# Kernel optimization log

Hardware: AMD Instinct MI355X
Metric: run time of the kernel (lower is better)

Reference implementation:

```python
import jax, jax.numpy as jnp
import numpy as np

TOPK = 13
NUM_CLASSES = 80
ALPHA = 1.0
BETA = 6.0
EPS = 1e-9
BS, NA, NMAX = 16, 8400, 64
IMG = 640


def _anchor_grid():
    pts = []
    for s in (8, 16, 32):
        n = IMG // s
        yv, xv = jnp.meshgrid(jnp.arange(n, dtype=jnp.float32), jnp.arange(n, dtype=jnp.float32), indexing='ij')
        pts.append(jnp.stack([(xv + 0.5) * s, (yv + 0.5) * s], -1).reshape(-1, 2))
    return jnp.concatenate(pts, 0)  # (8400, 2)


def setup_inputs() -> dict:
    key = jax.random.key(0)
    ks = jax.random.split(key, 6)
    pd_scores = jax.nn.sigmoid(jax.random.normal(ks[0], (BS, NA, NUM_CLASSES), jnp.float32))
    # predicted circles: centers in image, radii in [4, 68]
    pxy = jax.random.uniform(ks[1], (BS, NA, 2), jnp.float32) * IMG
    pr = jax.random.uniform(ks[1], (BS, NA, 1), jnp.float32) * 64.0 + 4.0
    pd_circles = jnp.concatenate([pxy, pr], -1)
    anc_points = _anchor_grid()
    gt_labels = jax.random.randint(ks[2], (BS, NMAX, 1), 0, NUM_CLASSES, jnp.int32)
    gxy = jax.random.uniform(ks[3], (BS, NMAX, 2), jnp.float32) * IMG
    gr = jax.random.uniform(ks[3], (BS, NMAX, 1), jnp.float32) * 64.0 + 8.0
    gt_bboxes = jnp.concatenate([gxy, gr], -1)  # circles (x, y, r)
    n_valid = jax.random.randint(ks[4], (BS, 1), 8, NMAX + 1)
    mask_gt = (jnp.arange(NMAX)[None, :] < n_valid).astype(jnp.float32)[..., None]
    return {"pd_scores": pd_scores, "pd_circles": pd_circles, "anc_points": anc_points,
            "gt_labels": gt_labels, "gt_bboxes": gt_bboxes, "mask_gt": mask_gt}


def circle_iou(c1, c2, eps):
    # c1, c2: broadcastable (..., 3) = (x, y, r); IoU of two discs via lens area.
    d = jnp.sqrt(jnp.sum((c1[..., :2] - c2[..., :2]) ** 2, -1) + eps)
    r1, r2 = c1[..., 2], c2[..., 2]
    a1, a2 = jnp.pi * r1 ** 2, jnp.pi * r2 ** 2
    cos1 = jnp.clip((d ** 2 + r1 ** 2 - r2 ** 2) / (2.0 * d * r1 + eps), -1.0, 1.0)
    cos2 = jnp.clip((d ** 2 + r2 ** 2 - r1 ** 2) / (2.0 * d * r2 + eps), -1.0, 1.0)
    tri = jnp.clip((r1 + r2 - d) * (d + r1 - r2) * (d - r1 + r2) * (d + r1 + r2), 0.0)
    lens = r1 ** 2 * jnp.arccos(cos1) + r2 ** 2 * jnp.arccos(cos2) - 0.5 * jnp.sqrt(tri)
    inter = jnp.where(d >= r1 + r2, 0.0,
                      jnp.where(d <= jnp.abs(r1 - r2), jnp.pi * jnp.minimum(r1, r2) ** 2, lens))
    return inter / (a1 + a2 - inter + eps)


def reference(pd_scores, pd_circles, anc_points, gt_labels, gt_bboxes, mask_gt):
    bs, na, nc = pd_scores.shape
    n_max = gt_bboxes.shape[1]
    # ---- candidates inside GT circles: (b, n_max, na) ----
    dist = jnp.linalg.norm(gt_bboxes[:, :, None, :2] - anc_points[None, None, :, :], axis=-1)
    mask_in_gts = (dist <= gt_bboxes[:, :, None, 2]).astype(jnp.float32)
    mask_valid = mask_in_gts * mask_gt  # mask_gt (b, n_max, 1) broadcasts
    # ---- alignment metric ----
    labels = jnp.clip(gt_labels[..., 0], 0, nc - 1)  # (b, n_max)
    b_idx = jnp.arange(bs)[:, None, None]
    a_idx = jnp.arange(na)[None, None, :]
    bbox_scores = pd_scores[b_idx, a_idx, labels[:, :, None]] * mask_valid  # (b, n_max, na)
    overlaps = circle_iou(gt_bboxes[:, :, None, :], pd_circles[:, None, :, :], EPS) * mask_valid
    align_metric = bbox_scores ** ALPHA * overlaps ** BETA
    # ---- topk candidate selection with duplicate suppression ----
    _, topk_idxs = jax.lax.top_k(align_metric, TOPK)  # (b, n_max, TOPK)
    topk_idxs = jnp.where(mask_gt > 0, topk_idxs, 0)
    count = jnp.zeros((bs, n_max, na), jnp.float32).at[
        jnp.arange(bs)[:, None, None], jnp.arange(n_max)[None, :, None], topk_idxs].add(1.0)
    mask_topk = jnp.where(count > 1, 0.0, count)
    mask_pos = mask_topk * mask_in_gts * mask_gt  # (b, n_max, na)
    # ---- resolve anchors claimed by multiple GTs via max overlap ----
    fg_count = mask_pos.sum(1)  # (b, na)
    is_max = jax.nn.one_hot(overlaps.argmax(1), n_max, axis=1, dtype=jnp.float32)  # (b, n_max, na)
    mask_pos = jnp.where(fg_count[:, None, :] > 1, is_max, mask_pos)
    fg_mask = mask_pos.sum(1)  # (b, na)
    target_gt_idx = mask_pos.argmax(1)  # (b, na)
    # ---- gather targets ----
    target_labels = jnp.clip(jnp.take_along_axis(gt_labels[..., 0], target_gt_idx, axis=1), 0, None)
    target_circles = jnp.take_along_axis(gt_bboxes, target_gt_idx[..., None], axis=1)  # (b, na, 3)
    target_scores = jax.nn.one_hot(target_labels, nc, dtype=pd_scores.dtype)
    target_scores = target_scores * (fg_mask[..., None] > 0)
    # ---- normalize scores by aligned metric ----
    align_metric = align_metric * mask_pos
    pos_align = jnp.max(align_metric, -1, keepdims=True)  # (b, n_max, 1)
    pos_overlaps = jnp.max(overlaps * mask_pos, -1, keepdims=True)
    norm = jnp.max(align_metric * pos_overlaps / (pos_align + EPS), 1)[..., None]  # (b, na, 1)
    target_scores = target_scores * norm
    return target_labels, target_circles, target_scores, fg_mask, target_gt_idx
```

## Files before the change

### kernel.cpp

```cpp
#include <hip/hip_runtime.h>
#include <cmath>

#define NA 8400
#define NC 80
#define BS 16
#define NMAX 64
#define TOPKK 13
#define CAP 768
#define CEPS 1e-9f
#define PIF 3.14159265358979323846f

#define OFF_LABELS  0
#define OFF_CIRCLES 134400
#define OFF_SCORES  537600
#define OFF_FG      11289600
#define OFF_TGI     11424000

#define WS_POSAL   1075200
#define WS_POSOV   1079296
#define WS_TGI     1083392
#define WS_ALIGN   1620992
#define ZERO1_F4   67712
#define ZERO2_F4   2688000

__device__ __forceinline__ float circle_iou_dev(float gx, float gy, float r1,
                                                float px, float py, float r2) {
    float dx = gx - px, dy = gy - py;
    float d = sqrtf(dx * dx + dy * dy + CEPS);
    float a1 = PIF * r1 * r1, a2 = PIF * r2 * r2;
    float d2 = d * d;
    float c1 = (d2 + r1 * r1 - r2 * r2) / (2.0f * d * r1 + CEPS);
    float c2 = (d2 + r2 * r2 - r1 * r1) / (2.0f * d * r2 + CEPS);
    c1 = fminf(fmaxf(c1, -1.0f), 1.0f);
    c2 = fminf(fmaxf(c2, -1.0f), 1.0f);
    float tri = fmaxf((r1 + r2 - d) * (d + r1 - r2) * (d - r1 + r2) * (d + r1 + r2), 0.0f);
    float lens = r1 * r1 * acosf(c1) + r2 * r2 * acosf(c2) - 0.5f * sqrtf(tri);
    float inter;
    if (d >= r1 + r2)             inter = 0.0f;
    else if (d <= fabsf(r1 - r2)) { float rm = fminf(r1, r2); inter = PIF * rm * rm; }
    else                          inter = lens;
    return inter / (a1 + a2 - inter + CEPS);
}

__global__ __launch_bounds__(256) void k0_zero(float4* __restrict__ wsz,
                                               float4* __restrict__ scores)
{
    int i = blockIdx.x * 256 + threadIdx.x;
    if (i < ZERO2_F4) scores[i] = make_float4(0.f, 0.f, 0.f, 0.f);
    else { int k = i - ZERO2_F4; if (k < ZERO1_F4) wsz[k] = make_float4(0.f, 0.f, 0.f, 0.f); }
}

__global__ __launch_bounds__(256) void k1_topk(
    const float* __restrict__ pd_scores, const float* __restrict__ pd_circles,
    const float* __restrict__ anc, const int* __restrict__ gt_labels,
    const float* __restrict__ gt_bboxes, const float* __restrict__ mask_gt,
    unsigned long long* __restrict__ colbits)
{
    __shared__ int   s_cidx[CAP];
    __shared__ float s_cval[CAP];
    __shared__ float s_low[64];
    __shared__ unsigned long long s_ingt0;
    __shared__ int   s_ncand, s_nsel, s_done;
    __shared__ float s_redv[4];
    __shared__ int   s_redi[4], s_redc[4];
    __shared__ int   s_sel[16];

    const int row = blockIdx.x;
    const int b = row >> 6, j = row & 63;
    const int t = threadIdx.x;
    const int lane = t & 63, wv = t >> 6;

    if (mask_gt[row] <= 0.0f) return;

    const float gx = gt_bboxes[row * 3 + 0];
    const float gy = gt_bboxes[row * 3 + 1];
    const float gr = gt_bboxes[row * 3 + 2];
    int lab = gt_labels[row];
    lab = min(max(lab, 0), NC - 1);

    if (t == 0) { s_ncand = 0; s_nsel = 0; s_done = 0; }
    if (t < 64) s_low[t] = 0.0f;
    __syncthreads();

    for (int k = 0; k < 33; ++k) {
        int a = k * 256 + t;
        bool in_gt = false;
        if (a < NA) {
            float ax = anc[2 * a], ay = anc[2 * a + 1];
            float dx = gx - ax, dy = gy - ay;
            in_gt = (sqrtf(dx * dx + dy * dy) <= gr);
        }
        if (in_gt) {
            int p = atomicAdd(&s_ncand, 1);
            if (p < CAP) s_cidx[p] = a;
        }
        if (k == 0 && wv == 0) {
            unsigned long long m = __ballot(in_gt);
            if (lane == 0) s_ingt0 = m;
        }
    }
    __syncthreads();
    const int n = min(s_ncand, CAP);

    for (int c = t; c < n; c += 256) {
        int a = s_cidx[c];
        size_t pi = (size_t)(b * NA + a);
        float px = pd_circles[pi * 3 + 0];
        float py = pd_circles[pi * 3 + 1];
        float pr = pd_circles[pi * 3 + 2];
        float iou = circle_iou_dev(gx, gy, gr, px, py, pr);
        float sc  = pd_scores[pi * NC + lab];
        float o2 = iou * iou;
        float v = sc * (o2 * o2 * o2);
        s_cval[c] = v;
        if (a < 64) s_low[a] = v;
    }
    __syncthreads();

    for (int it = 0; it < TOPKK; ++it) {
        float bv = -1.0f; int bi = 1 << 30, bc = -1;
        for (int c = t; c < n; c += 256) {
            float v = s_cval[c]; int a = s_cidx[c];
            if (v > bv || (v == bv && a < bi)) { bv = v; bi = a; bc = c; }
        }
        for (int off = 32; off > 0; off >>= 1) {
            float ov = __shfl_down(bv, off);
            int   oi = __shfl_down(bi, off);
            int   oc = __shfl_down(bc, off);
            if (ov > bv || (ov == bv && oi < bi)) { bv = ov; bi = oi; bc = oc; }
        }
        if (lane == 0) { s_redv[wv] = bv; s_redi[wv] = bi; s_redc[wv] = bc; }
        __syncthreads();
        if (t == 0) {
            float vb = s_redv[0]; int ib = s_redi[0], cb = s_redc[0];
            for (int w = 1; w < 4; ++w)
                if (s_redv[w] > vb || (s_redv[w] == vb && s_redi[w] < ib))
                    { vb = s_redv[w]; ib = s_redi[w]; cb = s_redc[w]; }
            if (vb > 0.0f) { s_sel[s_nsel] = ib; s_nsel++; s_cval[cb] = -1.0f; }
            else s_done = 1;
        }
        __syncthreads();
        if (s_done) break;
    }

    if (t == 0) {
        int r = TOPKK - s_nsel;
        if (r > 0) {
            for (int idx = 0; idx < 64 && r > 0; ++idx) {
                if (s_low[idx] > 0.0f) continue;
                r--;
                if ((s_ingt0 >> idx) & 1ull) { s_sel[s_nsel] = idx; s_nsel++; }
            }
        }
    }
    __syncthreads();

    if (t < s_nsel)
        atomicOr(&colbits[(size_t)b * NA + s_sel[t]], 1ull << j);
}

__global__ __launch_bounds__(256) void k2_resolve(
    const float* __restrict__ pd_scores, const float* __restrict__ pd_circles,
    const float* __restrict__ anc, const int* __restrict__ gt_labels,
    const float* __restrict__ gt_bboxes, const float* __restrict__ mask_gt,
    const unsigned long long* __restrict__ colbits,
    float* __restrict__ out, int* __restrict__ tgiE, float* __restrict__ alignv,
    unsigned int* __restrict__ posal, unsigned int* __restrict__ posov)
{
    const int idx = blockIdx.x * 256 + threadIdx.x;
    const int b = idx / NA;
    const int a = idx - b * NA;

    const unsigned long long col = colbits[idx];
    const int cnt = __popcll(col);

    int tgi = 0, fg = 0;
    if (cnt == 1) { fg = 1; tgi = __ffsll((unsigned long long)col) - 1; }
    else if (cnt > 1) {
        fg = 1;
        float px = pd_circles[(size_t)idx * 3 + 0];
        float py = pd_circles[(size_t)idx * 3 + 1];
        float pr = pd_circles[(size_t)idx * 3 + 2];
        float ax = anc[2 * a], ay = anc[2 * a + 1];
        float bo = -1.0f; int bj = 0;
        for (int j = 0; j < NMAX; ++j) {
            float mgv = mask_gt[b * NMAX + j];
            float gx = gt_bboxes[(b * NMAX + j) * 3 + 0];
            float gy = gt_bboxes[(b * NMAX + j) * 3 + 1];
            float gr = gt_bboxes[(b * NMAX + j) * 3 + 2];
            float ovj = 0.0f;
            if (mgv > 0.0f) {
                float dx = gx - ax, dy = gy - ay;
                if (sqrtf(dx * dx + dy * dy) <= gr)
                    ovj = circle_iou_dev(gx, gy, gr, px, py, pr);
            }
            if (ovj > bo) { bo = ovj; bj = j; }
        }
        tgi = bj;
    }

    const int gl = gt_labels[b * NMAX + tgi];
    const float gx = gt_bboxes[(b * NMAX + tgi) * 3 + 0];
    const float gy = gt_bboxes[(b * NMAX + tgi) * 3 + 1];
    const float gr = gt_bboxes[(b * NMAX + tgi) * 3 + 2];

    out[OFF_LABELS + idx] = (float)max(gl, 0);
    out[OFF_CIRCLES + (size_t)idx * 3 + 0] = gx;
    out[OFF_CIRCLES + (size_t)idx * 3 + 1] = gy;
    out[OFF_CIRCLES + (size_t)idx * 3 + 2] = gr;
    out[OFF_FG + idx]  = (float)fg;
    out[OFF_TGI + idx] = (float)tgi;
    tgiE[idx] = fg ? tgi : -1;

    float alg = 0.0f;
    if (fg) {
        float ovv = 0.0f;
        float mgv = mask_gt[b * NMAX + tgi];
        float ax = anc[2 * a], ay = anc[2 * a + 1];
        float dx = gx - ax, dy = gy - ay;
        if (mgv > 0.0f && sqrtf(dx * dx + dy * dy) <= gr) {
            float px = pd_circles[(size_t)idx * 3 + 0];
            float py = pd_circles[(size_t)idx * 3 + 1];
            float pr = pd_circles[(size_t)idx * 3 + 2];
            float iou = circle_iou_dev(gx, gy, gr, px, py, pr);
            int lab = min(max(gl, 0), NC - 1);
            float sc = pd_scores[((size_t)b * NA + a) * NC + lab];
            ovv = iou;
            float o2 = iou * iou;
            alg = sc * (o2 * o2 * o2);
        }
        atomicMax(&posal[b * NMAX + tgi], __float_as_uint(alg));
        atomicMax(&posov[b * NMAX + tgi], __float_as_uint(ovv));
    }
    alignv[idx] = alg;
}

__global__ __launch_bounds__(256) void k4_scatter(
    const int* __restrict__ tgiE, const float* __restrict__ alignv,
    const unsigned int* __restrict__ posal, const unsigned int* __restrict__ posov,
    const int* __restrict__ gt_labels, float* __restrict__ out)
{
    int idx = blockIdx.x * 256 + threadIdx.x;
    int tg = tgiE[idx];
    if (tg < 0) return;
    int b = idx / NA;
    float pa = __uint_as_float(posal[b * NMAX + tg]);
    float po = __uint_as_float(posov[b * NMAX + tg]);
    float norm = alignv[idx] * po / (pa + CEPS);
    int lab = max(gt_labels[b * NMAX + tg], 0);
    out[OFF_SCORES + (size_t)idx * NC + lab] = norm;
}

extern "C" void kernel_launch(void* const* d_in, const int* in_sizes, int n_in,
                              void* d_out, int out_size, void* d_ws, size_t ws_size,
                              hipStream_t stream) {
    const float* pd_scores  = (const float*)d_in[0];
    const float* pd_circles = (const float*)d_in[1];
    const float* anc        = (const float*)d_in[2];
    const int*   gt_labels  = (const int*)d_in[3];
    const float* gt_bboxes  = (const float*)d_in[4];
    const float* mask_gt    = (const float*)d_in[5];
    float* out = (float*)d_out;

    char* ws = (char*)d_ws;
    unsigned long long* colbits = (unsigned long long*)ws;
    unsigned int* posal = (unsigned int*)(ws + WS_POSAL);
    unsigned int* posov = (unsigned int*)(ws + WS_POSOV);
    int*   tgiE   = (int*)(ws + WS_TGI);
    float* alignv = (float*)(ws + WS_ALIGN);

    const int nz = ZERO2_F4 + ZERO1_F4;
    k0_zero<<<(nz + 255) / 256, 256, 0, stream>>>((float4*)ws,
                                                  (float4*)(out + OFF_SCORES));
    k1_topk<<<BS * NMAX, 256, 0, stream>>>(pd_scores, pd_circles, anc, gt_labels,
                                           gt_bboxes, mask_gt, colbits);
    k2_resolve<<<(BS * NA) / 256, 256, 0, stream>>>(pd_scores, pd_circles, anc,
                                                    gt_labels, gt_bboxes, mask_gt,
                                                    colbits, out, tgiE, alignv,
                                                    posal, posov);
    k4_scatter<<<(BS * NA) / 256, 256, 0, stream>>>(tgiE, alignv, posal, posov,
                                                    gt_labels, out);
}
```

Baseline: 165.3 us.

## Scan only anchor-grid cells near each GT and fuse score zeroing into scatter

The top-k kernel stops scanning all 8400 anchors per GT. It computes the bounding cell range on each of the three pyramid levels from the GT circle, generates anchor coordinates analytically, and evaluates only those cells, ordered by flattened cell index. The separate zeroing of the dense score tensor is removed, and the final kernel writes every float4 of the scores directly, either zero or the normalized value at the label slot. This cuts the per-GT anchor scan and one full pass of writes over the scores, but assumes the fixed anchor grid, and the tie-break order changes from anchor index to cell-list index.

After: 171.5 us. 1.04x slower.

```diff
diff --git a/kernel.cpp b/kernel.cpp
--- a/kernel.cpp
+++ b/kernel.cpp
@@ -6,7 +6,7 @@
 #define BS 16
 #define NMAX 64
 #define TOPKK 13
-#define CAP 768
+#define MAXCELL 768
 #define CEPS 1e-9f
 #define PIF 3.14159265358979323846f
 
@@ -21,7 +21,7 @@
 #define WS_TGI     1083392
 #define WS_ALIGN   1620992
 #define ZERO1_F4   67712
-#define ZERO2_F4   2688000
+#define NSC_F4     2688000
 
 __device__ __forceinline__ float circle_iou_dev(float gx, float gy, float r1,
                                                 float px, float py, float r2) {
@@ -42,27 +42,23 @@
     return inter / (a1 + a2 - inter + CEPS);
 }
 
-__global__ __launch_bounds__(256) void k0_zero(float4* __restrict__ wsz,
-                                               float4* __restrict__ scores)
+__global__ __launch_bounds__(256) void k0_zero(float4* __restrict__ wsz)
 {
     int i = blockIdx.x * 256 + threadIdx.x;
-    if (i < ZERO2_F4) scores[i] = make_float4(0.f, 0.f, 0.f, 0.f);
-    else { int k = i - ZERO2_F4; if (k < ZERO1_F4) wsz[k] = make_float4(0.f, 0.f, 0.f, 0.f); }
+    if (i < ZERO1_F4) wsz[i] = make_float4(0.f, 0.f, 0.f, 0.f);
 }
 
 __global__ __launch_bounds__(256) void k1_topk(
     const float* __restrict__ pd_scores, const float* __restrict__ pd_circles,
-    const float* __restrict__ anc, const int* __restrict__ gt_labels,
-    const float* __restrict__ gt_bboxes, const float* __restrict__ mask_gt,
-    unsigned long long* __restrict__ colbits)
+    const int* __restrict__ gt_labels, const float* __restrict__ gt_bboxes,
+    const float* __restrict__ mask_gt, unsigned long long* __restrict__ colbits)
 {
-    __shared__ int   s_cidx[CAP];
-    __shared__ float s_cval[CAP];
+    __shared__ float s_val[MAXCELL];
     __shared__ float s_low[64];
     __shared__ unsigned long long s_ingt0;
-    __shared__ int   s_ncand, s_nsel, s_done;
+    __shared__ int   s_nsel, s_done;
     __shared__ float s_redv[4];
-    __shared__ int   s_redi[4], s_redc[4];
+    __shared__ int   s_redi[4];
     __shared__ int   s_sel[16];
 
     const int row = blockIdx.x;
@@ -78,66 +74,96 @@
     int lab = gt_labels[row];
     lab = min(max(lab, 0), NC - 1);
 
-    if (t == 0) { s_ncand = 0; s_nsel = 0; s_done = 0; }
+    if (t == 0) { s_nsel = 0; s_done = 0; }
     if (t < 64) s_low[t] = 0.0f;
+
+    int c0_0, r0_0, w_0, c0_1, r0_1, w_1, c0_2, r0_2, w_2;
+    int off1, off2, tot;
+    {
+        float inv = 0.125f;
+        c0_0 = max(0, (int)floorf((gx - gr) * inv - 0.5f) - 1);
+        int c1 = min(79, (int)ceilf((gx + gr) * inv - 0.5f) + 1);
+        r0_0 = max(0, (int)floorf((gy - gr) * inv - 0.5f) - 1);
+        int r1 = min(79, (int)ceilf((gy + gr) * inv - 0.5f) + 1);
+        w_0 = max(0, c1 - c0_0 + 1); int h0 = max(0, r1 - r0_0 + 1);
+        inv = 0.0625f;
+        c0_1 = max(0, (int)floorf((gx - gr) * inv - 0.5f) - 1);
+        c1 = min(39, (int)ceilf((gx + gr) * inv - 0.5f) + 1);
+        r0_1 = max(0, (int)floorf((gy - gr) * inv - 0.5f) - 1);
+        r1 = min(39, (int)ceilf((gy + gr) * inv - 0.5f) + 1);
+        w_1 = max(0, c1 - c0_1 + 1); int h1 = max(0, r1 - r0_1 + 1);
+        inv = 0.03125f;
+        c0_2 = max(0, (int)floorf((gx - gr) * inv - 0.5f) - 1);
+        c1 = min(19, (int)ceilf((gx + gr) * inv - 0.5f) + 1);
+        r0_2 = max(0, (int)floorf((gy - gr) * inv - 0.5f) - 1);
+        r1 = min(19, (int)ceilf((gy + gr) * inv - 0.5f) + 1);
+        w_2 = max(0, c1 - c0_2 + 1); int h2 = max(0, r1 - r0_2 + 1);
+        off1 = w_0 * h0;
+        off2 = off1 + w_1 * h1;
+        tot  = min(off2 + w_2 * h2, MAXCELL);
+    }
+
+    if (wv == 0) {
+        float ax = ((float)lane + 0.5f) * 8.0f;
+        float dx = gx - ax, dy = gy - 4.0f;
+        bool ig = (sqrtf(dx * dx + dy * dy) <= gr);
+        unsigned long long m = __ballot(ig);
+        if (lane == 0) s_ingt0 = m;
+    }
     __syncthreads();
 
-    for (int k = 0; k < 33; ++k) {
-        int a = k * 256 + t;
-        bool in_gt = false;
-        if (a < NA) {
-            float ax = anc[2 * a], ay = anc[2 * a + 1];
-            float dx = gx - ax, dy = gy - ay;
-            in_gt = (sqrtf(dx * dx + dy * dy) <= gr);
-        }
-        if (in_gt) {
-            int p = atomicAdd(&s_ncand, 1);
-            if (p < CAP) s_cidx[p] = a;
-        }
-        if (k == 0 && wv == 0) {
-            unsigned long long m = __ballot(in_gt);
-            if (lane == 0) s_ingt0 = m;
-        }
+    for (int i = t; i < tot; i += 256) {
+        int rr, cc, base, nlev; float s;
+        if (i < off1)      { int l = i;        rr = r0_0 + l / w_0; cc = c0_0 + l % w_0; base = 0;    nlev = 80; s = 8.0f;  }
+        else if (i < off2) { int l = i - off1; rr = r0_1 + l / w_1; cc = c0_1 + l % w_1; base = 6400; nlev = 40; s = 16.0f; }
+        else               { int l = i - off2; rr = r0_2 + l / w_2; cc = c0_2 + l % w_2; base = 8000; nlev = 20; s = 32.0f; }
+        float ax = ((float)cc + 0.5f) * s;
+        float ay = ((float)rr + 0.5f) * s;
+        float dx = gx - ax, dy = gy - ay;
+        float v = 0.0f;
+        int a = base + rr * nlev + cc;
+        if (sqrtf(dx * dx + dy * dy) <= gr) {
+            size_t pi = (size_t)(b * NA + a);
+            float px = pd_circles[pi * 3 + 0];
+            float py = pd_circles[pi * 3 + 1];
+            float pr = pd_circles[pi * 3 + 2];
+            float iou = circle_iou_dev(gx, gy, gr, px, py, pr);
+            float sc  = pd_scores[pi * NC + lab];
+            float o2 = iou * iou;
+            v = sc * (o2 * o2 * o2);
+        }
+        s_val[i] = v;
+        if (a < 64) s_low[a] = v;
     }
     __syncthreads();
-    const int n = min(s_ncand, CAP);
-
-    for (int c = t; c < n; c += 256) {
-        int a = s_cidx[c];
-        size_t pi = (size_t)(b * NA + a);
-        float px = pd_circles[pi * 3 + 0];
-        float py = pd_circles[pi * 3 + 1];
-        float pr = pd_circles[pi * 3 + 2];
-        float iou = circle_iou_dev(gx, gy, gr, px, py, pr);
-        float sc  = pd_scores[pi * NC + lab];
-        float o2 = iou * iou;
-        float v = sc * (o2 * o2 * o2);
-        s_cval[c] = v;
-        if (a < 64) s_low[a] = v;
-    }
-    __syncthreads();
 
     for (int it = 0; it < TOPKK; ++it) {
-        float bv = -1.0f; int bi = 1 << 30, bc = -1;
-        for (int c = t; c < n; c += 256) {
-            float v = s_cval[c]; int a = s_cidx[c];
-            if (v > bv || (v == bv && a < bi)) { bv = v; bi = a; bc = c; }
+        float bv = -1.0f; int bi = 1 << 30;
+        for (int i = t; i < tot; i += 256) {
+            float v = s_val[i];
+            if (v > bv || (v == bv && i < bi)) { bv = v; bi = i; }
         }
         for (int off = 32; off > 0; off >>= 1) {
             float ov = __shfl_down(bv, off);
             int   oi = __shfl_down(bi, off);
-            int   oc = __shfl_down(bc, off);
-            if (ov > bv || (ov == bv && oi < bi)) { bv = ov; bi = oi; bc = oc; }
-        }
-        if (lane == 0) { s_redv[wv] = bv; s_redi[wv] = bi; s_redc[wv] = bc; }
+            if (ov > bv || (ov == bv && oi < bi)) { bv = ov; bi = oi; }
+        }
+        if (lane == 0) { s_redv[wv] = bv; s_redi[wv] = bi; }
         __syncthreads();
         if (t == 0) {
-            float vb = s_redv[0]; int ib = s_redi[0], cb = s_redc[0];
+            float vb = s_redv[0]; int ib = s_redi[0];
             for (int w = 1; w < 4; ++w)
                 if (s_redv[w] > vb || (s_redv[w] == vb && s_redi[w] < ib))
-                    { vb = s_redv[w]; ib = s_redi[w]; cb = s_redc[w]; }
-            if (vb > 0.0f) { s_sel[s_nsel] = ib; s_nsel++; s_cval[cb] = -1.0f; }
-            else s_done = 1;
+                    { vb = s_redv[w]; ib = s_redi[w]; }
+            if (vb > 0.0f) {
+                int rr, cc, base, nlev;
+                if (ib < off1)      { int l = ib;        rr = r0_0 + l / w_0; cc = c0_0 + l % w_0; base = 0;    nlev = 80; }
+                else if (ib < off2) { int l = ib - off1; rr = r0_1 + l / w_1; cc = c0_1 + l % w_1; base = 6400; nlev = 40; }
+                else                { int l = ib - off2; rr = r0_2 + l / w_2; cc = c0_2 + l % w_2; base = 8000; nlev = 20; }
+                s_sel[s_nsel] = base + rr * nlev + cc;
+                s_nsel++;
+                s_val[ib] = -1.0f;
+            } else s_done = 1;
         }
         __syncthreads();
         if (s_done) break;
@@ -235,20 +261,27 @@
     alignv[idx] = alg;
 }
 
-__global__ __launch_bounds__(256) void k4_scatter(
+__global__ __launch_bounds__(256) void k3_scores(
     const int* __restrict__ tgiE, const float* __restrict__ alignv,
     const unsigned int* __restrict__ posal, const unsigned int* __restrict__ posov,
-    const int* __restrict__ gt_labels, float* __restrict__ out)
+    const int* __restrict__ gt_labels, float4* __restrict__ scores)
 {
-    int idx = blockIdx.x * 256 + threadIdx.x;
-    int tg = tgiE[idx];
-    if (tg < 0) return;
-    int b = idx / NA;
-    float pa = __uint_as_float(posal[b * NMAX + tg]);
-    float po = __uint_as_float(posov[b * NMAX + tg]);
-    float norm = alignv[idx] * po / (pa + CEPS);
-    int lab = max(gt_labels[b * NMAX + tg], 0);
-    out[OFF_SCORES + (size_t)idx * NC + lab] = norm;
+    const int i = blockIdx.x * 256 + threadIdx.x;
+    const int anchor = i / 20;
+    const int q = i - anchor * 20;
+    float4 v = make_float4(0.f, 0.f, 0.f, 0.f);
+    const int tg = tgiE[anchor];
+    if (tg >= 0) {
+        const int b = anchor / NA;
+        const int lab = max(gt_labels[b * NMAX + tg], 0);
+        if ((lab >> 2) == q) {
+            float pa = __uint_as_float(posal[b * NMAX + tg]);
+            float po = __uint_as_float(posov[b * NMAX + tg]);
+            float norm = alignv[anchor] * po / (pa + CEPS);
+            ((float*)&v)[lab & 3] = norm;
+        }
+    }
+    scores[i] = v;
 }
 
 extern "C" void kernel_launch(void* const* d_in, const int* in_sizes, int n_in,
@@ -269,15 +302,14 @@
     int*   tgiE   = (int*)(ws + WS_TGI);
     float* alignv = (float*)(ws + WS_ALIGN);
 
-    const int nz = ZERO2_F4 + ZERO1_F4;
-    k0_zero<<<(nz + 255) / 256, 256, 0, stream>>>((float4*)ws,
-                                                  (float4*)(out + OFF_SCORES));
-    k1_topk<<<BS * NMAX, 256, 0, stream>>>(pd_scores, pd_circles, anc, gt_labels,
+    k0_zero<<<(ZERO1_F4 + 255) / 256, 256, 0, stream>>>((float4*)ws);
+    k1_topk<<<BS * NMAX, 256, 0, stream>>>(pd_scores, pd_circles, gt_labels,
                                            gt_bboxes, mask_gt, colbits);
     k2_resolve<<<(BS * NA) / 256, 256, 0, stream>>>(pd_scores, pd_circles, anc,
                                                     gt_labels, gt_bboxes, mask_gt,
                                                     colbits, out, tgiE, alignv,
                                                     posal, posov);
-    k4_scatter<<<(BS * NA) / 256, 256, 0, stream>>>(tgiE, alignv, posal, posov,
-                                                    gt_labels, out);
-}
+    k3_scores<<<NSC_F4 / 256, 256, 0, stream>>>(tgiE, alignv, posal, posov,
+                                                gt_labels,
+                                                (float4*)(out + OFF_SCORES));
+}
```
